# Kernel optimization log

Hardware: AMD Instinct MI355X
Metric: run time of the kernel (lower is better)

The kernel has to match this reference:

```python
import jax, jax.numpy as jnp
import numpy as np

N, E, DIN, HID, G, L = 50000, 200000, 128, 128, 64, 6
H1, H2 = 8, 4
EPS_LN, EPS_BN = 1e-5, 1e-5


def setup_inputs() -> dict:
    key = jax.random.key(0)
    ks = iter(jax.random.split(key, 32))
    def nrm(shape, scale=0.05):
        return jax.random.normal(next(ks), shape, dtype=jnp.float32) * scale
    z = lambda *s: jnp.zeros(s, jnp.float32)
    o = lambda *s: jnp.ones(s, jnp.float32)
    return {
        'x': jax.random.normal(next(ks), (N, DIN), dtype=jnp.float32),
        'edge_index': jax.random.randint(next(ks), (2, E), 0, N),
        'batch': jnp.sort(jax.random.randint(next(ks), (N,), 0, G)),
        'W1': nrm((DIN, H1 * HID)), 'a_src1': nrm((H1, HID)), 'a_dst1': nrm((H1, HID)), 'b1': z(H1 * HID),
        'W2': nrm((H1 * HID, H2 * HID)), 'a_src2': nrm((H2, HID)), 'a_dst2': nrm((H2, HID)), 'b2': z(H2 * HID),
        'W3': nrm((H2 * HID, HID)), 'b3': z(HID),
        'wq': nrm((L, HID, HID)), 'bq': z(L, HID), 'wk': nrm((L, HID, HID)), 'bk': z(L, HID),
        'wv': nrm((L, HID, HID)), 'bv': z(L, HID), 'wo': nrm((L, HID, HID)), 'bo': z(L, HID),
        'ln1g': o(L, HID), 'ln1b': z(L, HID), 'ln2g': o(L, HID), 'ln2b': z(L, HID),
        'wf1': nrm((L, HID, 4 * HID)), 'bf1': z(L, 4 * HID), 'wf2': nrm((L, 4 * HID, HID)), 'bf2': z(L, HID),
        'bn1_g': o(2 * HID), 'bn1_b': z(2 * HID),
        'fc1_w': nrm((2 * HID, HID // 2)), 'fc1_b': z(HID // 2),
        'bn2_g': o(HID // 2), 'bn2_b': z(HID // 2),
        'fc2_w': nrm((HID // 2, 2)), 'fc2_b': z(2),
    }


def _ln(x, g, b):
    mu = x.mean(-1, keepdims=True)
    v = ((x - mu) ** 2).mean(-1, keepdims=True)
    return (x - mu) * jax.lax.rsqrt(v + EPS_LN) * g + b


def _gat(x, src, dst, W, a_s, a_d, b, heads):
    # PyG GATConv: message src -> dst, segment softmax over incoming edges per dst.
    h = (x @ W).reshape(x.shape[0], heads, -1)           # [N, H, C]
    e = jax.nn.leaky_relu((h * a_s).sum(-1)[src] + (h * a_d).sum(-1)[dst], 0.2)  # [E, H]
    m = jax.ops.segment_max(e, dst, num_segments=N)
    ex = jnp.exp(e - jnp.where(jnp.isfinite(m), m, 0.0)[dst])
    s = jax.ops.segment_sum(ex, dst, num_segments=N)
    alpha = ex / (s[dst] + 1e-16)
    out = jax.ops.segment_sum(alpha[:, :, None] * h[src], dst, num_segments=N)
    return out.reshape(N, -1) + b


def _forward(x, edge_index, batch, W1, a_src1, a_dst1, b1, W2, a_src2, a_dst2, b2, W3, b3,
             wq, bq, wk, bk, wv, bv, wo, bo, ln1g, ln1b, ln2g, ln2b, wf1, bf1, wf2, bf2,
             bn1_g, bn1_b, fc1_w, fc1_b, bn2_g, bn2_b, fc2_w, fc2_b):
    loop = jnp.arange(N, dtype=edge_index.dtype)
    src = jnp.concatenate([edge_index[0], loop])          # add self-loops (PyG default)
    dst = jnp.concatenate([edge_index[1], loop])
    h = jax.nn.elu(_gat(x, src, dst, W1, a_src1, a_dst1, b1, H1))
    h = jax.nn.elu(_gat(h, src, dst, W2, a_src2, a_dst2, b2, H2))
    # GCNConv with symmetric normalization (self-loops already included)
    deg = jax.ops.segment_sum(jnp.ones(src.shape, h.dtype), dst, num_segments=N)
    dinv = jnp.where(deg > 0, jax.lax.rsqrt(jnp.maximum(deg, 1e-12)), 0.0)
    norm = dinv[src] * dinv[dst]
    h = jax.nn.elu(jax.ops.segment_sum(norm[:, None] * (h @ W3)[src], dst, num_segments=N) + b3)
    # TransformerEncoder over seq_len=1 (h3.unsqueeze(1)): softmax over one key == 1,
    # so MHA output == Wo @ (Wv h + bv) + bo exactly; q/k have no effect on the output.
    for l in range(L):
        sa = (h @ wv[l] + bv[l]) @ wo[l] + bo[l]
        h = _ln(h + sa, ln1g[l], ln1b[l])
        ff = jax.nn.gelu(h @ wf1[l] + bf1[l], approximate=False) @ wf2[l] + bf2[l]
        h = _ln(h + ff, ln2g[l], ln2b[l])
    # global mean / max pool over graphs
    cnt = jax.ops.segment_sum(jnp.ones((N,), h.dtype), batch, num_segments=G)
    hm = jax.ops.segment_sum(h, batch, num_segments=G) / jnp.maximum(cnt, 1.0)[:, None]
    hx = jax.ops.segment_max(h, batch, num_segments=G)
    hx = jnp.where(jnp.isfinite(hx), hx, 0.0)
    hc = jnp.concatenate([hm, hx], axis=1)                # [G, 2*HID]
    bn_s = 1.0 / np.sqrt(1.0 + EPS_BN)                    # eval BN: running stats (0, 1)
    hc = hc * bn_s * bn1_g + bn1_b
    hc = jax.nn.elu(hc @ fc1_w + fc1_b)
    hc = hc * bn_s * bn2_g + bn2_b
    return hc @ fc2_w + fc2_b                             # [G, 2]


def reference(x, edge_index, batch, W1, a_src1, a_dst1, b1, W2, a_src2, a_dst2, b2, W3, b3,
              wq, bq, wk, bk, wv, bv, wo, bo, ln1g, ln1b, ln2g, ln2b, wf1, bf1, wf2, bf2,
              bn1_g, bn1_b, fc1_w, fc1_b, bn2_g, bn2_b, fc2_w, fc2_b):
    return _forward(x, edge_index, batch, W1, a_src1, a_dst1, b1, W2, a_src2, a_dst2, b2, W3, b3,
                    wq, bq, wk, bk, wv, bv, wo, bo, ln1g, ln1b, ln2g, ln2b, wf1, bf1, wf2, bf2,
                    bn1_g, bn1_b, fc1_w, fc1_b, bn2_g, bn2_b, fc2_w, fc2_b)
```

## Files before the change

### kernel.cpp

```cpp
#include <hip/hip_runtime.h>
#include <hip/hip_bf16.h>
#include <math.h>

#define NN 50000
#define EE 200000
#define ET 250000
#define GG 64
#define LL 6

using short8 = __attribute__((ext_vector_type(8))) short;
using f32x4  = __attribute__((ext_vector_type(4))) float;
typedef unsigned short ushortT;

__device__ __forceinline__ float elu1(float x) { return x > 0.f ? x : expm1f(x); }
__device__ __forceinline__ float gelu_exact(float x) {
    return 0.5f * x * (1.f + erff(x * 0.70710678118654752440f));
}
__device__ __forceinline__ short f2bf(float f) {
    __hip_bfloat16 h = __float2bfloat16(f);
    return *reinterpret_cast<short*>(&h);
}
__device__ __forceinline__ float bf2f(ushortT u) {
    return __uint_as_float(((unsigned)u) << 16);
}

__global__ void count_deg_kernel(const int* __restrict__ ei, int* __restrict__ deg) {
    int e = blockIdx.x * 256 + threadIdx.x;
    if (e >= ET) return;
    int dst = (e < EE) ? ei[EE + e] : (e - EE);
    atomicAdd(&deg[dst], 1);
}

__global__ void scan_kernel(const int* __restrict__ deg, int* __restrict__ row_ptr, int n) {
    __shared__ int s[1024];
    int tid = threadIdx.x;
    const int per = (n + 1023) / 1024;
    int lo = tid * per, hi = min(lo + per, n);
    int sum = 0;
    for (int i = lo; i < hi; i++) sum += deg[i];
    s[tid] = sum;
    __syncthreads();
    for (int off = 1; off < 1024; off <<= 1) {
        int t = (tid >= off) ? s[tid - off] : 0;
        __syncthreads();
        s[tid] += t;
        __syncthreads();
    }
    int run = s[tid] - sum;
    for (int i = lo; i < hi; i++) { row_ptr[i] = run; run += deg[i]; }
    if (tid == 1023) row_ptr[n] = s[1023];
}

__global__ void fill_csr_kernel(const int* __restrict__ ei, const int* __restrict__ row_ptr,
                                int* __restrict__ cursor, int* __restrict__ edge_src) {
    int e = blockIdx.x * 256 + threadIdx.x;
    if (e >= ET) return;
    int src, dst;
    if (e < EE) { src = ei[e]; dst = ei[EE + e]; }
    else        { src = e - EE; dst = e - EE; }
    int pos = atomicAdd(&cursor[dst], 1);
    edge_src[row_ptr[dst] + pos] = src;
}

__global__ void dinv_kernel(const int* __restrict__ row_ptr, float* __restrict__ dinv) {
    int n = blockIdx.x * 256 + threadIdx.x;
    if (n >= NN) return;
    int d = row_ptr[n + 1] - row_ptr[n];
    dinv[n] = (d > 0) ? rsqrtf((float)d) : 0.f;
}

__global__ void wvwo_kernel(const float* __restrict__ wv, const float* __restrict__ wo,
                            const float* __restrict__ bv, const float* __restrict__ bo,
                            float* __restrict__ Wvo, float* __restrict__ bvo) {
    int l = blockIdx.y;
    const float* Wv = wv + l * 16384;
    const float* Wo = wo + l * 16384;
    int tid = blockIdx.x * 256 + threadIdx.x;
    if (tid < 16384) {
        int r = tid >> 7, c = tid & 127;
        float s = 0.f;
        for (int k = 0; k < 128; k++) s += Wv[r * 128 + k] * Wo[k * 128 + c];
        Wvo[l * 16384 + tid] = s;
    }
    if (blockIdx.x == 0 && threadIdx.x < 128) {
        int c = threadIdx.x;
        float s = bo[l * 128 + c];
        for (int k = 0; k < 128; k++) s += bv[l * 128 + k] * Wo[k * 128 + c];
        bvo[l * 128 + c] = s;
    }
}

__global__ void bprep_kernel(const float* __restrict__ B, short* __restrict__ Bp,
                             int K, int N, int ldb, long srcStride) {
    int layer = blockIdx.y;
    const float* Bsrc = B + srcStride * layer;
    short* Bd = Bp + (size_t)K * N * layer;
    int total = (K >> 5) * (N >> 4) * 64;
    int tid = blockIdx.x * 256 + threadIdx.x;
    if (tid >= total) return;
    int l = tid & 63;
    int rest = tid >> 6;
    int kbc = K >> 5;
    int kb = rest % kbc;
    int c16 = rest / kbc;
    int n = c16 * 16 + (l & 15);
    int kbase = kb * 32 + (l >> 4) * 8;
    short v[8];
#pragma unroll
    for (int j = 0; j < 8; j++) v[j] = f2bf(Bsrc[(size_t)(kbase + j) * ldb + n]);
    *(uint4*)(Bd + (size_t)tid * 8) = *(uint4*)v;
}

__global__ void cast_bf16_kernel(const float* __restrict__ in, short* __restrict__ out, int n4) {
    int i = blockIdx.x * 256 + threadIdx.x;
    if (i >= n4) return;
    float4 v = *(const float4*)(in + (size_t)i * 4);
    short s[4] = { f2bf(v.x), f2bf(v.y), f2bf(v.z), f2bf(v.w) };
    *(uint2*)(out + (size_t)i * 4) = *(uint2*)s;
}

template <int EPI, bool BIAS, bool OUTBF16, int NSPLIT, int KBC>
__global__ __launch_bounds__(256) void gemm_bf16_kernel(
    const short* __restrict__ A, const short* __restrict__ Bp,
    const float* __restrict__ bias, void* __restrict__ Cv,
    const float* __restrict__ a_s, const float* __restrict__ a_d,
    float* __restrict__ as_out, float* __restrict__ ad_out, int asH,
    const ushortT* __restrict__ Rres, const float* __restrict__ lng,
    const float* __restrict__ lnb, float* __restrict__ Qout,
    __hip_bfloat16* __restrict__ Qbout,
    int M, int K, int Nc) {
    __shared__ short Bs[(KBC > 0) ? KBC * 4096 : 8192];
    int t = threadIdx.x;
    int w = t >> 6, l = t & 63;
    int ln = l & 15, lq = l >> 4;
    int MBceil = (M + 63) >> 6;
    int bx = blockIdx.x;
    int xcd = bx & 7, idx = bx >> 3;
    int t2 = idx % NSPLIT;
    int mb = (idx / NSPLIT) * 8 + xcd;
    if (mb >= MBceil) return;
    int bm = mb * 64 + w * 16;
    int arow = bm + ln;
    bool aok = arow < M;
    int rowb = bm + lq * 4;
    const short* Ap = A + (size_t)arow * K + lq * 8;

    f32x4 acc[8];
#pragma unroll
    for (int j = 0; j < 8; j++) acc[j] = (f32x4){0.f, 0.f, 0.f, 0.f};

    if constexpr (KBC > 0) {
        {
            const uint4* src = (const uint4*)(Bp + (size_t)t2 * KBC * 4096);
            uint4* dst = (uint4*)Bs;
#pragma unroll
            for (int i = 0; i < KBC * 2; i++)
                dst[i * 256 + t] = src[i * 256 + t];
        }
        short8 af[KBC];
#pragma unroll
        for (int kb = 0; kb < KBC; kb++)
            af[kb] = aok ? *(const short8*)(Ap + kb * 32) : (short8){0,0,0,0,0,0,0,0};
        __syncthreads();
#pragma unroll
        for (int kb = 0; kb < KBC; kb++)
#pragma unroll
            for (int ct = 0; ct < 8; ct++) {
                short8 bfr = *(const short8*)(Bs + ((ct * KBC + kb) * 64 + l) * 8);
                acc[ct] = __builtin_amdgcn_mfma_f32_16x16x32_bf16(af[kb], bfr, acc[ct], 0, 0, 0);
            }
    } else {
        int kbc = K >> 5;
        int sct = t >> 5, spart = t & 31;
        auto stage = [&](int buf, int kb) {
            const uint4* src = (const uint4*)(Bp + ((size_t)(t2 * 8 + sct) * kbc + kb) * 512);
            uint4* dst = (uint4*)(Bs + buf * 4096 + sct * 512);
            dst[spart * 2]     = src[spart * 2];
            dst[spart * 2 + 1] = src[spart * 2 + 1];
        };
        stage(0, 0);
        __syncthreads();
        for (int kb = 0; kb < kbc; kb++) {
            if (kb + 1 < kbc) stage((kb + 1) & 1, kb + 1);
            short8 af = aok ? *(const short8*)(Ap + kb * 32) : (short8){0,0,0,0,0,0,0,0};
            const short* bsb = Bs + (kb & 1) * 4096;
#pragma unroll
            for (int ct = 0; ct < 8; ct++) {
                short8 bfr = *(const short8*)(bsb + (ct * 64 + l) * 8);
                acc[ct] = __builtin_amdgcn_mfma_f32_16x16x32_bf16(af, bfr, acc[ct], 0, 0, 0);
            }
            __syncthreads();
        }
    }

    if (EPI == 2) {
        const float* asv = a_s + t2 * 128;
        const float* adv = a_d + t2 * 128;
#pragma unroll
        for (int reg = 0; reg < 4; reg++) {
            float vs = 0.f, vd = 0.f;
#pragma unroll
            for (int ct = 0; ct < 8; ct++) {
                int colL = ct * 16 + ln;
                float av = acc[ct][reg];
                vs += av * asv[colL];
                vd += av * adv[colL];
            }
            vs += __shfl_xor(vs, 1); vs += __shfl_xor(vs, 2);
            vs += __shfl_xor(vs, 4); vs += __shfl_xor(vs, 8);
            vd += __shfl_xor(vd, 1); vd += __shfl_xor(vd, 2);
            vd += __shfl_xor(vd, 4); vd += __shfl_xor(vd, 8);
            int row = rowb + reg;
            if (ln == 0 && row < M) {
                as_out[(size_t)row * asH + t2] = vs;
                ad_out[(size_t)row * asH + t2] = vd;
            }
        }
    }
    if (EPI == 3) {
        float v[8][4];
#pragma unroll
        for (int ct = 0; ct < 8; ct++) {
            int col = ct * 16 + ln;
            float bv_ = bias[col];
#pragma unroll
            for (int reg = 0; reg < 4; reg++) {
                int row = rowb + reg;
                float r = (row < M) ? bf2f(Rres[(size_t)row * 128 + col]) : 0.f;
                v[ct][reg] = acc[ct][reg] + bv_ + r;
            }
        }
#pragma unroll
        for (int reg = 0; reg < 4; reg++) {
            float s = 0.f;
#pragma unroll
            for (int ct = 0; ct < 8; ct++) s += v[ct][reg];
            s += __shfl_xor(s, 1); s += __shfl_xor(s, 2);
            s += __shfl_xor(s, 4); s += __shfl_xor(s, 8);
            float mean = s * (1.f / 128.f);
            float s2 = 0.f;
#pragma unroll
            for (int ct = 0; ct < 8; ct++) { float d = v[ct][reg] - mean; s2 += d * d; }
            s2 += __shfl_xor(s2, 1); s2 += __shfl_xor(s2, 2);
            s2 += __shfl_xor(s2, 4); s2 += __shfl_xor(s2, 8);
            float rstd = rsqrtf(s2 * (1.f / 128.f) + 1e-5f);
            int row = rowb + reg;
            if (row < M) {
#pragma unroll
                for (int ct = 0; ct < 8; ct++) {
                    int col = ct * 16 + ln;
                    float o = (v[ct][reg] - mean) * rstd * lng[col] + lnb[col];
                    Qbout[(size_t)row * 128 + col] = __float2bfloat16(o);
                    if (Qout) Qout[(size_t)row * 128 + col] = o;
                }
            }
        }
    }
    if (EPI == 0 || EPI == 1 || EPI == 2) {
#pragma unroll
        for (int ct = 0; ct < 8; ct++) {
            int col = t2 * 128 + ct * 16 + ln;
            float bv_ = BIAS ? bias[col] : 0.f;
#pragma unroll
            for (int reg = 0; reg < 4; reg++) {
                int row = rowb + reg;
                if (row < M) {
                    float v = acc[ct][reg] + bv_;
                    if (EPI == 1) v = gelu_exact(v);
                    if (OUTBF16)
                        ((__hip_bfloat16*)Cv)[(size_t)row * Nc + col] = __float2bfloat16(v);
                    else
                        ((float*)Cv)[(size_t)row * Nc + col] = v;
                }
            }
        }
    }
}

template <int H>
__global__ __launch_bounds__(256) void gat_agg_fused_kernel(
    const ushortT* __restrict__ hpre, const float* __restrict__ as_,
    const float* __restrict__ ad_, const float* __restrict__ bias,
    const int* __restrict__ row_ptr, const int* __restrict__ edge_src,
    __hip_bfloat16* __restrict__ out, int n_nodes) {
    const int CPT = H;
    int node = blockIdx.x * 2 + (threadIdx.x >> 7);
    if (node >= n_nodes) return;
    int tt = threadIdx.x & 127;
    int c0 = tt * CPT;
    int hb = c0 >> 7;
    int start = row_ptr[node];
    int deg = row_ptr[node + 1] - start;
    float adn = ad_[(size_t)node * H + hb];
    float m = -1e30f, S = 0.f;
    float acc[CPT];
#pragma unroll
    for (int c = 0; c < CPT; c++) acc[c] = 0.f;
    for (int j = 0; j < deg; j++) {
        int s = edge_src[start + j];
        float e = as_[(size_t)s * H + hb] + adn;
        e = e > 0.f ? e : 0.2f * e;
        float mn = fmaxf(m, e);
        float sc = expf(m - mn);
        float wj = expf(e - mn);
        S = S * sc + wj;
        const ushortT* hp = hpre + (size_t)s * (H * 128) + c0;
        float hv[CPT];
        if (CPT == 8) {
            uint4 u = *(const uint4*)hp;
            hv[0] = bf2f((ushortT)(u.x & 0xffff)); hv[1] = bf2f((ushortT)(u.x >> 16));
            hv[2] = bf2f((ushortT)(u.y & 0xffff)); hv[3] = bf2f((ushortT)(u.y >> 16));
            hv[4] = bf2f((ushortT)(u.z & 0xffff)); hv[5] = bf2f((ushortT)(u.z >> 16));
            hv[6] = bf2f((ushortT)(u.w & 0xffff)); hv[7] = bf2f((ushortT)(u.w >> 16));
        } else {
            uint2 u = *(const uint2*)hp;
            hv[0] = bf2f((ushortT)(u.x & 0xffff)); hv[1] = bf2f((ushortT)(u.x >> 16));
            hv[2] = bf2f((ushortT)(u.y & 0xffff)); hv[3] = bf2f((ushortT)(u.y >> 16));
        }
#pragma unroll
        for (int c = 0; c < CPT; c++) acc[c] = acc[c] * sc + wj * hv[c];
        m = mn;
    }
    float inv = 1.f / (S + 1e-16f);
#pragma unroll
    for (int c = 0; c < CPT; c++)
        out[(size_t)node * (H * 128) + c0 + c] =
            __float2bfloat16(elu1(acc[c] * inv + bias[c0 + c]));
}

__global__ __launch_bounds__(256) void gcn_agg_kernel(
    const ushortT* __restrict__ hp, const float* __restrict__ dinv,
    const float* __restrict__ b3, const int* __restrict__ row_ptr,
    const int* __restrict__ edge_src,
    __hip_bfloat16* __restrict__ outb, int n_nodes) {
    int node = blockIdx.x * 2 + (threadIdx.x >> 7);
    int c = threadIdx.x & 127;
    if (node >= n_nodes) return;
    int start = row_ptr[node];
    int deg = row_ptr[node + 1] - start;
    float dn = dinv[node];
    float acc = 0.f;
    for (int j = 0; j < deg; j++) {
        int s = edge_src[start + j];
        acc += dinv[s] * dn * bf2f(hp[(size_t)s * 128 + c]);
    }
    outb[(size_t)node * 128 + c] = __float2bfloat16(elu1(acc + b3[c]));
}

__global__ void pool1_kernel(const float* __restrict__ Q, const int* __restrict__ batch,
                             float* __restrict__ psum, float* __restrict__ pmax, int n_nodes) {
    int g = blockIdx.x, seg = blockIdx.y;
    int c = threadIdx.x;
    int lo, hi;
    {
        int l = 0, h = n_nodes;
        while (l < h) { int mid = (l + h) >> 1; if (batch[mid] < g) l = mid + 1; else h = mid; }
        lo = l;
        l = lo; h = n_nodes;
        while (l < h) { int mid = (l + h) >> 1; if (batch[mid] < g + 1) l = mid + 1; else h = mid; }
        hi = l;
    }
    int len = hi - lo;
    int a = lo + (int)((long)len * seg / 8);
    int b = lo + (int)((long)len * (seg + 1) / 8);
    float s = 0.f, mx = -INFINITY;
    for (int n = a; n < b; n++) {
        float v = Q[(size_t)n * 128 + c];
        s += v;
        mx = fmaxf(mx, v);
    }
    psum[(g * 8 + seg) * 128 + c] = s;
    pmax[(g * 8 + seg) * 128 + c] = mx;
}

__global__ void pool2_kernel(const float* __restrict__ psum, const float* __restrict__ pmax,
                             const int* __restrict__ batch,
                             const float* __restrict__ bn1g, const float* __restrict__ bn1b,
                             float* __restrict__ hc, int n_nodes) {
    int g = blockIdx.x;
    int c = threadIdx.x;
    int lo, hi;
    {
        int l = 0, h = n_nodes;
        while (l < h) { int mid = (l + h) >> 1; if (batch[mid] < g) l = mid + 1; else h = mid; }
        lo = l;
        l = lo; h = n_nodes;
        while (l < h) { int mid = (l + h) >> 1; if (batch[mid] < g + 1) l = mid + 1; else h = mid; }
        hi = l;
    }
    int cnt = hi - lo;
    float s = 0.f, mx = -INFINITY;
    for (int seg = 0; seg < 8; seg++) {
        s += psum[(g * 8 + seg) * 128 + c];
        mx = fmaxf(mx, pmax[(g * 8 + seg) * 128 + c]);
    }
    float hm = s / fmaxf((float)cnt, 1.f);
    float hx = (cnt > 0 && isfinite(mx)) ? mx : 0.f;
    const float bn_s = 0.99999500003749968f;
    hc[g * 256 + c]       = hm * bn_s * bn1g[c] + bn1b[c];
    hc[g * 256 + 128 + c] = hx * bn_s * bn1g[128 + c] + bn1b[128 + c];
}

__global__ void head_kernel(const float* __restrict__ hc,
                            const float* __restrict__ fc1w, const float* __restrict__ fc1b,
                            const float* __restrict__ bn2g, const float* __restrict__ bn2b,
                            const float* __restrict__ fc2w, const float* __restrict__ fc2b,
                            float* __restrict__ out) {
    int g = blockIdx.x;
    int j = threadIdx.x;
    const float bn_s = 0.99999500003749968f;
    float acc = fc1b[j];
    for (int i = 0; i < 256; i++) acc += hc[g * 256 + i] * fc1w[i * 64 + j];
    acc = elu1(acc);
    acc = acc * bn_s * bn2g[j] + bn2b[j];
    __shared__ float sv[64];
    sv[j] = acc;
    __syncthreads();
    if (j < 2) {
        float o = fc2b[j];
        for (int i = 0; i < 64; i++) o += sv[i] * fc2w[i * 2 + j];
        out[g * 2 + j] = o;
    }
}

extern "C" void kernel_launch(void* const* d_in, const int* in_sizes, int n_in,
                              void* d_out, int out_size, void* d_ws, size_t ws_size,
                              hipStream_t stream) {
    const float* x    = (const float*)d_in[0];
    const int*   ei   = (const int*)d_in[1];
    const int*   batch= (const int*)d_in[2];
    const float* W1   = (const float*)d_in[3];
    const float* as1  = (const float*)d_in[4];
    const float* ad1  = (const float*)d_in[5];
    const float* b1   = (const float*)d_in[6];
    const float* W2   = (const float*)d_in[7];
    const float* as2  = (const float*)d_in[8];
    const float* ad2  = (const float*)d_in[9];
    const float* b2   = (const float*)d_in[10];
    const float* W3   = (const float*)d_in[11];
    const float* b3   = (const float*)d_in[12];
    const float* wv   = (const float*)d_in[17];
    const float* bv   = (const float*)d_in[18];
    const float* wo   = (const float*)d_in[19];
    const float* bo   = (const float*)d_in[20];
    const float* ln1g = (const float*)d_in[21];
    const float* ln1b = (const float*)d_in[22];
    const float* ln2g = (const float*)d_in[23];
    const float* ln2b = (const float*)d_in[24];
    const float* wf1  = (const float*)d_in[25];
    const float* bf1  = (const float*)d_in[26];
    const float* wf2  = (const float*)d_in[27];
    const float* bf2  = (const float*)d_in[28];
    const float* bn1g = (const float*)d_in[29];
    const float* bn1b = (const float*)d_in[30];
    const float* fc1w = (const float*)d_in[31];
    const float* fc1b = (const float*)d_in[32];
    const float* bn2g = (const float*)d_in[33];
    const float* bn2b = (const float*)d_in[34];
    const float* fc2w = (const float*)d_in[35];
    const float* fc2b = (const float*)d_in[36];
    float* out = (float*)d_out;

    char* wsb = (char*)d_ws;
    short* xb    = (short*)wsb;
    short* h1pre = (short*)(wsb + 12800000);
    short* h2pre = (short*)(wsb + 12800000);
    short* h3pre = (short*)(wsb + 12800000);
    short* FFb   = (short*)(wsb + 25600000);
    short* bh1   = (short*)(wsb + 115200000);
    short* bh2   = (short*)(wsb + 115200000);
    float* fQ    = (float*)(wsb + 128000000);
    short* Qb    = (short*)(wsb + 153600000);
    char* tail = wsb + 217600000;
    short* W1p  = (short*)tail;  tail += 262144;
    short* W2p  = (short*)tail;  tail += 1048576;
    short* W3p  = (short*)tail;  tail += 131072;
    short* Wvop = (short*)tail;  tail += 196608;
    short* wf1p = (short*)tail;  tail += 786432;
    short* wf2p = (short*)tail;  tail += 786432;
    float* Wvo  = (float*)tail;  tail += 393216;
    float* bvo  = (float*)tail;  tail += 3072;
    float* fAS  = (float*)tail;  tail += 1600000;
    float* fAD  = (float*)tail;  tail += 1600000;
    float* fDv  = (float*)tail;  tail += 200000;
    float* psum = (float*)tail;  tail += 262144;
    float* pmax = (float*)tail;  tail += 262144;
    float* fHC  = (float*)tail;  tail += 65536;
    int* iDeg   = (int*)tail;    tail += 200000;
    int* iRP    = (int*)tail;    tail += 200004;
    int* iCur   = (int*)tail;    tail += 200000;
    int* iES    = (int*)tail;    tail += 1000000;

    hipMemsetAsync(iDeg, 0, NN * sizeof(int), stream);
    hipMemsetAsync(iCur, 0, NN * sizeof(int), stream);

    count_deg_kernel<<<(ET + 255) / 256, 256, 0, stream>>>(ei, iDeg);
    scan_kernel<<<1, 1024, 0, stream>>>(iDeg, iRP, NN);
    fill_csr_kernel<<<(ET + 255) / 256, 256, 0, stream>>>(ei, iRP, iCur, iES);
    dinv_kernel<<<(NN + 255) / 256, 256, 0, stream>>>(iRP, fDv);

    wvwo_kernel<<<dim3(64, 6), 256, 0, stream>>>(wv, wo, bv, bo, Wvo, bvo);
    auto bprep = [&](const float* B, short* Bp, int K, int N, int ldb, long sStride, int layers) {
        int total = (K >> 5) * (N >> 4) * 64;
        dim3 grid((total + 255) / 256, layers);
        bprep_kernel<<<grid, 256, 0, stream>>>(B, Bp, K, N, ldb, sStride);
    };
    bprep(W1, W1p, 128, 1024, 1024, 0, 1);
    bprep(W2, W2p, 1024, 512, 512, 0, 1);
    bprep(W3, W3p, 512, 128, 128, 0, 1);
    bprep(Wvo, Wvop, 128, 128, 128, 16384, 6);
    bprep(wf1, wf1p, 128, 512, 512, 65536, 6);
    bprep(wf2, wf2p, 512, 128, 128, 65536, 6);
    cast_bf16_kernel<<<(NN * 128 / 4 + 255) / 256, 256, 0, stream>>>(x, xb, NN * 128 / 4);

    const int MB64 = (NN + 63) / 64;
    const int MBp = ((MB64 + 7) / 8) * 8;

    gemm_bf16_kernel<2, false, true, 8, 4><<<MBp * 8, 256, 0, stream>>>(
        xb, W1p, nullptr, h1pre, as1, ad1, fAS, fAD, 8,
        nullptr, nullptr, nullptr, nullptr, nullptr, NN, 128, 1024);
    gat_agg_fused_kernel<8><<<(NN + 1) / 2, 256, 0, stream>>>(
        (const ushortT*)h1pre, fAS, fAD, b1, iRP, iES, (__hip_bfloat16*)bh1, NN);
    gemm_bf16_kernel<2, false, true, 4, 0><<<MBp * 4, 256, 0, stream>>>(
        bh1, W2p, nullptr, h2pre, as2, ad2, fAS, fAD, 4,
        nullptr, nullptr, nullptr, nullptr, nullptr, NN, 1024, 512);
    gat_agg_fused_kernel<4><<<(NN + 1) / 2, 256, 0, stream>>>(
        (const ushortT*)h2pre, fAS, fAD, b2, iRP, iES, (__hip_bfloat16*)bh2, NN);
    gemm_bf16_kernel<0, false, true, 1, 0><<<MBp, 256, 0, stream>>>(
        bh2, W3p, nullptr, h3pre, nullptr, nullptr, nullptr, nullptr, 0,
        nullptr, nullptr, nullptr, nullptr, nullptr, NN, 512, 128);
    gcn_agg_kernel<<<(NN + 1) / 2, 256, 0, stream>>>(
        (const ushortT*)h3pre, fDv, b3, iRP, iES, (__hip_bfloat16*)Qb, NN);
    for (int l = 0; l < LL; l++) {
        gemm_bf16_kernel<3, true, false, 1, 4><<<MBp, 256, 0, stream>>>(
            Qb, Wvop + l * 16384, bvo + l * 128, nullptr, nullptr, nullptr, nullptr, nullptr, 0,
            (const ushortT*)Qb, ln1g + l * 128, ln1b + l * 128, nullptr, (__hip_bfloat16*)Qb,
            NN, 128, 128);
        gemm_bf16_kernel<1, true, true, 4, 4><<<MBp * 4, 256, 0, stream>>>(
            Qb, wf1p + l * 65536, bf1 + l * 512, FFb, nullptr, nullptr, nullptr, nullptr, 0,
            nullptr, nullptr, nullptr, nullptr, nullptr, NN, 128, 512);
        gemm_bf16_kernel<3, true, false, 1, 0><<<MBp, 256, 0, stream>>>(
            FFb, wf2p + l * 65536, bf2 + l * 128, nullptr, nullptr, nullptr, nullptr, nullptr, 0,
            (const ushortT*)Qb, ln2g + l * 128, ln2b + l * 128,
            (l == LL - 1) ? fQ : nullptr, (__hip_bfloat16*)Qb, NN, 512, 128);
    }
    pool1_kernel<<<dim3(GG, 8), 128, 0, stream>>>(fQ, batch, psum, pmax, NN);
    pool2_kernel<<<GG, 128, 0, stream>>>(psum, pmax, batch, bn1g, bn1b, fHC, NN);
    head_kernel<<<GG, 64, 0, stream>>>(fHC, fc1w, fc1b, bn2g, bn2b, fc2w, fc2b, out);
}
```

Measured before the change: 1.346 ms.

## Split GAT aggregation into precomputed softmax weights and weighted gather pass

Replaces the fused online-softmax GAT aggregation with two kernels: one computes per-edge exponentiated attention scores and per-node sums using wavefront-parallel max/sum reductions, and a second accumulates weighted neighbor features and normalizes. This removes the redundant exp and rescaling work that every channel thread repeated per edge. In exchange, it adds a kernel launch and a write/read of the per-edge weight buffer, which reuses workspace space.

```diff
diff --git a/kernel.cpp b/kernel.cpp
--- a/kernel.cpp
+++ b/kernel.cpp
@@ -278,9 +278,48 @@
 }
 
 template <int H>
-__global__ __launch_bounds__(256) void gat_agg_fused_kernel(
-    const ushortT* __restrict__ hpre, const float* __restrict__ as_,
-    const float* __restrict__ ad_, const float* __restrict__ bias,
+__global__ __launch_bounds__(256) void gat_alpha_kernel(
+    const float* __restrict__ as_, const float* __restrict__ ad_,
+    const int* __restrict__ row_ptr, const int* __restrict__ edge_src,
+    float* __restrict__ exA, float* __restrict__ exS, int n_nodes) {
+    const int GS = 64 / H;
+    int node = blockIdx.x * 4 + (threadIdx.x >> 6);
+    if (node >= n_nodes) return;
+    int l = threadIdx.x & 63;
+    int h = l / GS;
+    int lig = l % GS;
+    int start = row_ptr[node];
+    int deg = row_ptr[node + 1] - start;
+    float adn = ad_[(size_t)node * H + h];
+    float m = -1e30f;
+    for (int j = lig; j < deg; j += GS) {
+        int s = edge_src[start + j];
+        float e = as_[(size_t)s * H + h] + adn;
+        e = e > 0.f ? e : 0.2f * e;
+        m = fmaxf(m, e);
+    }
+#pragma unroll
+    for (int mask = 1; mask < GS; mask <<= 1)
+        m = fmaxf(m, __shfl_xor(m, mask));
+    float S = 0.f;
+    for (int j = lig; j < deg; j += GS) {
+        int s = edge_src[start + j];
+        float e = as_[(size_t)s * H + h] + adn;
+        e = e > 0.f ? e : 0.2f * e;
+        float ex = expf(e - m);
+        exA[(size_t)(start + j) * H + h] = ex;
+        S += ex;
+    }
+#pragma unroll
+    for (int mask = 1; mask < GS; mask <<= 1)
+        S += __shfl_xor(S, mask);
+    if (lig == 0) exS[(size_t)node * H + h] = S;
+}
+
+template <int H>
+__global__ __launch_bounds__(256) void gat_agg2_kernel(
+    const ushortT* __restrict__ hpre, const float* __restrict__ exA,
+    const float* __restrict__ exS, const float* __restrict__ bias,
     const int* __restrict__ row_ptr, const int* __restrict__ edge_src,
     __hip_bfloat16* __restrict__ out, int n_nodes) {
     const int CPT = H;
@@ -291,19 +330,12 @@
     int hb = c0 >> 7;
     int start = row_ptr[node];
     int deg = row_ptr[node + 1] - start;
-    float adn = ad_[(size_t)node * H + hb];
-    float m = -1e30f, S = 0.f;
     float acc[CPT];
 #pragma unroll
     for (int c = 0; c < CPT; c++) acc[c] = 0.f;
     for (int j = 0; j < deg; j++) {
         int s = edge_src[start + j];
-        float e = as_[(size_t)s * H + hb] + adn;
-        e = e > 0.f ? e : 0.2f * e;
-        float mn = fmaxf(m, e);
-        float sc = expf(m - mn);
-        float wj = expf(e - mn);
-        S = S * sc + wj;
+        float a = exA[(size_t)(start + j) * H + hb];
         const ushortT* hp = hpre + (size_t)s * (H * 128) + c0;
         float hv[CPT];
         if (CPT == 8) {
@@ -318,10 +350,9 @@
             hv[2] = bf2f((ushortT)(u.y & 0xffff)); hv[3] = bf2f((ushortT)(u.y >> 16));
         }
 #pragma unroll
-        for (int c = 0; c < CPT; c++) acc[c] = acc[c] * sc + wj * hv[c];
-        m = mn;
-    }
-    float inv = 1.f / (S + 1e-16f);
+        for (int c = 0; c < CPT; c++) acc[c] += a * hv[c];
+    }
+    float inv = 1.f / (exS[(size_t)node * H + hb] + 1e-16f);
 #pragma unroll
     for (int c = 0; c < CPT; c++)
         out[(size_t)node * (H * 128) + c0 + c] =
@@ -463,6 +494,8 @@
 
     char* wsb = (char*)d_ws;
     short* xb    = (short*)wsb;
+    float* exAf  = (float*)wsb;
+    float* exSf  = (float*)(wsb + 8000000);
     short* h1pre = (short*)(wsb + 12800000);
     short* h2pre = (short*)(wsb + 12800000);
     short* h3pre = (short*)(wsb + 12800000);
@@ -519,13 +552,17 @@
     gemm_bf16_kernel<2, false, true, 8, 4><<<MBp * 8, 256, 0, stream>>>(
         xb, W1p, nullptr, h1pre, as1, ad1, fAS, fAD, 8,
         nullptr, nullptr, nullptr, nullptr, nullptr, NN, 128, 1024);
-    gat_agg_fused_kernel<8><<<(NN + 1) / 2, 256, 0, stream>>>(
-        (const ushortT*)h1pre, fAS, fAD, b1, iRP, iES, (__hip_bfloat16*)bh1, NN);
+    gat_alpha_kernel<8><<<(NN + 3) / 4, 256, 0, stream>>>(
+        fAS, fAD, iRP, iES, exAf, exSf, NN);
+    gat_agg2_kernel<8><<<(NN + 1) / 2, 256, 0, stream>>>(
+        (const ushortT*)h1pre, exAf, exSf, b1, iRP, iES, (__hip_bfloat16*)bh1, NN);
     gemm_bf16_kernel<2, false, true, 4, 0><<<MBp * 4, 256, 0, stream>>>(
         bh1, W2p, nullptr, h2pre, as2, ad2, fAS, fAD, 4,
         nullptr, nullptr, nullptr, nullptr, nullptr, NN, 1024, 512);
-    gat_agg_fused_kernel<4><<<(NN + 1) / 2, 256, 0, stream>>>(
-        (const ushortT*)h2pre, fAS, fAD, b2, iRP, iES, (__hip_bfloat16*)bh2, NN);
+    gat_alpha_kernel<4><<<(NN + 3) / 4, 256, 0, stream>>>(
+        fAS, fAD, iRP, iES, exAf, exSf, NN);
+    gat_agg2_kernel<4><<<(NN + 1) / 2, 256, 0, stream>>>(
+        (const ushortT*)h2pre, exAf, exSf, b2, iRP, iES, (__hip_bfloat16*)bh2, NN);
     gemm_bf16_kernel<0, false, true, 1, 0><<<MBp, 256, 0, stream>>>(
         bh2, W3p, nullptr, h3pre, nullptr, nullptr, nullptr, nullptr, 0,
         nullptr, nullptr, nullptr, nullptr, nullptr, NN, 512, 128);
```

Result: no change. 1.364 ms (+1.3%).
